# Kernel optimization log

Hardware: AMD Instinct MI355X
Metric: run time of the kernel (lower is better)

Reference implementation:

```python
import jax, jax.numpy as jnp
import numpy as np

B, S, D_IN, D_OUT = 4, 2048, 1024, 1024


def setup_inputs() -> dict:
    key = jax.random.key(0)
    kx, kq, kk, kv = jax.random.split(key, 4)
    scale = 1.0 / np.sqrt(D_IN)
    return {
        "x": jax.random.normal(kx, (B, S, D_IN), dtype=jnp.float32),
        "W_q": jax.random.normal(kq, (D_IN, D_OUT), dtype=jnp.float32) * scale,
        "W_k": jax.random.normal(kk, (D_IN, D_OUT), dtype=jnp.float32) * scale,
        "W_v": jax.random.normal(kv, (D_IN, D_OUT), dtype=jnp.float32) * scale,
    }


def reference(x, W_q, W_k, W_v):
    # QKV projections (Linear without bias): [B,S,D_out]
    q = jnp.einsum("bsd,de->bse", x, W_q)
    k = jnp.einsum("bsd,de->bse", x, W_k)
    v = jnp.einsum("bsd,de->bse", x, W_v)

    # Raw scores [B,S,S], causal mask (strict upper triangle -> -inf),
    # then scale by sqrt(d_k) and softmax, matching the torch order of ops.
    scores = jnp.einsum("bqd,bkd->bqk", q, k)
    seq = scores.shape[-1]
    causal = jnp.triu(jnp.ones((seq, seq), dtype=bool), k=1)
    scores = jnp.where(causal[None, :, :], -jnp.inf, scores)
    attn = jax.nn.softmax(scores / jnp.sqrt(jnp.asarray(q.shape[-1], scores.dtype)), axis=-1)
    # dropout p=0.0 -> identity (eval semantics)
    return jnp.einsum("bqk,bkd->bqd", attn, v)
```

## Files before the change

### kernel.cpp

```cpp
#include <hip/hip_runtime.h>

typedef unsigned short u16;
typedef __bf16 bf16x8 __attribute__((ext_vector_type(8)));
typedef float f32x4 __attribute__((ext_vector_type(4)));

__device__ __forceinline__ u16 f2bf(float f) {
    union { float f; unsigned int u; } v; v.f = f;
    unsigned int u = v.u;
    return (u16)((u + 0x7FFFu + ((u >> 16) & 1u)) >> 16);
}
__device__ __forceinline__ float bf2f(u16 h) {
    union { unsigned int u; float f; } v; v.u = ((unsigned int)h) << 16;
    return v.f;
}

__device__ __forceinline__ void load_lds16(const void* g, void* l) {
    __builtin_amdgcn_global_load_lds(
        (const __attribute__((address_space(1))) unsigned int*)g,
        (__attribute__((address_space(3))) unsigned int*)l,
        16, 0, 0);
}

__global__ void __launch_bounds__(256) cast_x_kernel(const float4* __restrict__ X,
                                                     u16* __restrict__ out) {
    int idx = blockIdx.x * 256 + threadIdx.x;
    float4 v = X[idx];
    ushort4 o;
    o.x = f2bf(v.x); o.y = f2bf(v.y); o.z = f2bf(v.z); o.w = f2bf(v.w);
    *(ushort4*)(out + (size_t)idx * 4) = o;
}

__global__ void __launch_bounds__(256) transpose_w_kernel(
    const float* __restrict__ W0, const float* __restrict__ W1, const float* __restrict__ W2,
    u16* __restrict__ O0, u16* __restrict__ O1, u16* __restrict__ O2) {
    const float* W = (blockIdx.z == 0) ? W0 : (blockIdx.z == 1) ? W1 : W2;
    u16* O = (blockIdx.z == 0) ? O0 : (blockIdx.z == 1) ? O1 : O2;
    __shared__ float tile[32][33];
    int tx = threadIdx.x, ty = threadIdx.y;
    int n0 = blockIdx.x * 32, k0 = blockIdx.y * 32;
    #pragma unroll
    for (int j = 0; j < 32; j += 8)
        tile[ty + j][tx] = W[(size_t)(k0 + ty + j) * 1024 + n0 + tx];
    __syncthreads();
    #pragma unroll
    for (int j = 0; j < 32; j += 8)
        O[(size_t)(n0 + ty + j) * 1024 + k0 + tx] = f2bf(tile[tx][ty + j]);
}

template <int MODE>
__global__ void __launch_bounds__(256) gemm_nt(
    const u16* __restrict__ A, const u16* __restrict__ Bq,
    const u16* __restrict__ Bk, const u16* __restrict__ Bv,
    void* __restrict__ Cq, void* __restrict__ Ck, void* __restrict__ Cv,
    float* __restrict__ rowsum,
    int N, int K, long sA, long sB, long sC, float cscale) {
    int mtile, ntile, z;
    if (MODE == 0) {
        int L = blockIdx.x;
        int c = L & 7, t = (L >> 3) & 7, hi = L >> 6;
        int p = hi * 8 + c;
        z = p >> 6; mtile = p & 63; ntile = t;
    } else if (MODE == 1) {
        int c = blockIdx.x & 7, g = blockIdx.x >> 3;
        z = blockIdx.z;
        if (g <= c)               { mtile = c;     ntile = g; }
        else if (g < 2 * c + 10)  { mtile = c + 8; ntile = g - (c + 1); }
        else return;
    } else {
        int L = blockIdx.x;
        int c = L & 7, x = (L >> 3) & 7, hi = L >> 6;
        int p = hi * 8 + c;
        z = p >> 4; mtile = p & 15; ntile = x;
    }

    const u16* B;
    if (MODE == 0) {
        B = (z == 0) ? Bq : (z == 1) ? Bk : Bv;
    } else {
        B = Bq + (size_t)z * sB;
        A += (size_t)z * sA;
    }

    __shared__ __align__(16) u16 As[2][128 * 32];
    __shared__ __align__(16) u16 Bs[2][128 * 32];

    const int tid = threadIdx.x;
    const int lane = tid & 63;
    const int wave = tid >> 6;
    const int wr = wave >> 1, wc = wave & 1;

    int kiters = K >> 6;
    if (MODE == 3) kiters = (mtile + 1) * 2;

    const int r0 = tid >> 2;
    const int kb = (((tid & 3) ^ ((r0 >> 1) & 3))) * 16;

    const char* gA0 = (const char*)(A + (size_t)(mtile * 128 + r0) * K) + kb;
    const char* gA1 = gA0 + (size_t)64 * K * 2;
    const char* gB0 = (const char*)(B + (size_t)(ntile * 128 + r0) * K) + kb;
    const char* gB1 = gB0 + (size_t)64 * K * 2;

    char* lA = (char*)(&As[0][0]) + tid * 16;
    char* lB = (char*)(&Bs[0][0]) + tid * 16;

    f32x4 acc[4][4] = {};

    const int quad = lane >> 4;
    const int l16 = lane & 15;
    const int ch = quad ^ ((l16 >> 1) & 3);
    const int aoff = (wr * 64 + l16) * 32 + ch * 8;
    const int boff = (wc * 64 + l16) * 32 + ch * 8;

    for (int kt = 0; kt < kiters; ++kt) {
        load_lds16(gA0,      lA);
        load_lds16(gA1,      lA + 4096);
        load_lds16(gA0 + 64, lA + 8192);
        load_lds16(gA1 + 64, lA + 12288);
        load_lds16(gB0,      lB);
        load_lds16(gB1,      lB + 4096);
        load_lds16(gB0 + 64, lB + 8192);
        load_lds16(gB1 + 64, lB + 12288);
        gA0 += 128; gA1 += 128; gB0 += 128; gB1 += 128;
        __syncthreads();

        #pragma unroll
        for (int h = 0; h < 2; ++h) {
            const u16* ap = &As[h][aoff];
            const u16* bp = &Bs[h][boff];
            bf16x8 af[4], bfv[4];
            #pragma unroll
            for (int r = 0; r < 4; ++r) af[r] = *(const bf16x8*)(ap + r * 512);
            #pragma unroll
            for (int c = 0; c < 4; ++c) bfv[c] = *(const bf16x8*)(bp + c * 512);
            #pragma unroll
            for (int r = 0; r < 4; ++r)
                #pragma unroll
                for (int c = 0; c < 4; ++c)
                    acc[r][c] = __builtin_amdgcn_mfma_f32_16x16x32_bf16(af[r], bfv[c], acc[r][c], 0, 0, 0);
        }
        __syncthreads();
    }

    const int grow0 = mtile * 128 + wr * 64 + quad * 4;
    const int gcol0 = ntile * 128 + wc * 64 + l16;

    if (MODE == 0) {
        if (z < 2) {
            u16* C = (u16*)((z == 0) ? Cq : Ck);
            #pragma unroll
            for (int r = 0; r < 4; ++r)
                #pragma unroll
                for (int c = 0; c < 4; ++c)
                    #pragma unroll
                    for (int i = 0; i < 4; ++i)
                        C[(size_t)(grow0 + r * 16 + i) * N + gcol0 + c * 16] =
                            f2bf(acc[r][c][i]);
        } else {
            u16* C = (u16*)Cv;
            #pragma unroll
            for (int r = 0; r < 4; ++r) {
                int m0 = grow0 + r * 16;
                int b = m0 >> 11, s0 = m0 & 2047;
                #pragma unroll
                for (int c = 0; c < 4; ++c) {
                    int d = gcol0 + c * 16;
                    ushort4 o;
                    o.x = f2bf(acc[r][c][0]); o.y = f2bf(acc[r][c][1]);
                    o.z = f2bf(acc[r][c][2]); o.w = f2bf(acc[r][c][3]);
                    *(ushort4*)(C + (size_t)b * (1024 * 2048) + (size_t)d * 2048 + s0) = o;
                }
            }
        }
    } else if (MODE == 1) {
        u16* C = (u16*)Cq + (size_t)z * sC;
        float* rs = rowsum + z * 2048;
        const bool diag = (ntile == mtile);
        float rsum[4][4];
        #pragma unroll
        for (int r = 0; r < 4; ++r)
            #pragma unroll
            for (int i = 0; i < 4; ++i) rsum[r][i] = 0.f;
        #pragma unroll
        for (int r = 0; r < 4; ++r)
            #pragma unroll
            for (int c = 0; c < 4; ++c)
                #pragma unroll
                for (int i = 0; i < 4; ++i) {
                    int grow = grow0 + r * 16 + i;
                    int gcol = gcol0 + c * 16;
                    float e = 0.f;
                    if (!diag || gcol <= grow)
                        e = __expf(acc[r][c][i] * cscale - 12.0f);
                    C[(size_t)grow * N + gcol] = f2bf(e);
                    rsum[r][i] += e;
                }
        #pragma unroll
        for (int r = 0; r < 4; ++r)
            #pragma unroll
            for (int i = 0; i < 4; ++i) {
                float s = rsum[r][i];
                s += __shfl_xor(s, 1, 64);
                s += __shfl_xor(s, 2, 64);
                s += __shfl_xor(s, 4, 64);
                s += __shfl_xor(s, 8, 64);
                if (l16 == 0)
                    atomicAdd(&rs[grow0 + r * 16 + i], s);
            }
    } else {
        float* C = (float*)Cq + (size_t)z * sC;
        const float* rs = rowsum + z * 2048;
        #pragma unroll
        for (int r = 0; r < 4; ++r)
            #pragma unroll
            for (int i = 0; i < 4; ++i) {
                int grow = grow0 + r * 16 + i;
                float inv = 1.0f / rs[grow];
                #pragma unroll
                for (int c = 0; c < 4; ++c)
                    C[(size_t)grow * N + gcol0 + c * 16] = acc[r][c][i] * inv;
            }
    }
}

extern "C" void kernel_launch(void* const* d_in, const int* in_sizes, int n_in,
                              void* d_out, int out_size, void* d_ws, size_t ws_size,
                              hipStream_t stream) {
    const float* x  = (const float*)d_in[0];
    const float* Wq = (const float*)d_in[1];
    const float* Wk = (const float*)d_in[2];
    const float* Wv = (const float*)d_in[3];
    float* out = (float*)d_out;
    char* ws = (char*)d_ws;
    const size_t Mi = 1u << 20;

    u16* xb  = (u16*)(ws);
    u16* WqT = (u16*)(ws + 16 * Mi);
    u16* WkT = (u16*)(ws + 18 * Mi);
    u16* WvT = (u16*)(ws + 20 * Mi);
    u16* Q   = (u16*)(ws + 22 * Mi);
    u16* Kb  = (u16*)(ws + 38 * Mi);
    u16* Vt  = (u16*)(ws + 54 * Mi);
    u16* S   = (u16*)(ws + 70 * Mi);
    float* rowsum = (float*)(ws + 16 * Mi);

    cast_x_kernel<<<8192, 256, 0, stream>>>((const float4*)x, xb);
    transpose_w_kernel<<<dim3(32, 32, 3), dim3(32, 8), 0, stream>>>(
        Wq, Wk, Wv, WqT, WkT, WvT);

    gemm_nt<0><<<dim3(1536, 1, 1), 256, 0, stream>>>(
        xb, WqT, WkT, WvT, Q, Kb, Vt, nullptr, 1024, 1024, 0, 0, 0, 1.f);

    hipMemsetAsync(rowsum, 0, 4 * 2048 * sizeof(float), stream);

    gemm_nt<1><<<dim3(192, 1, 4), 256, 0, stream>>>(
        Q, Kb, nullptr, nullptr, S, nullptr, nullptr, rowsum, 2048, 1024,
        (long)2048 * 1024, (long)2048 * 1024, (long)2048 * 2048, 0.03125f);

    gemm_nt<3><<<dim3(512, 1, 1), 256, 0, stream>>>(
        S, Vt, nullptr, nullptr, out, nullptr, nullptr, rowsum, 1024, 2048,
        (long)2048 * 2048, (long)1024 * 2048, (long)2048 * 1024, 1.f);
}
```

Baseline: 237.5 us.

## Fuse prep kernels, move V projection into QK stage, compute rowsums via MFMA

Merges the x cast and weight transpose into one launch. The V projection moves out of the QK projection launch and into the score launch, which balances work across launches. The atomic rowsum accumulation and its memset are replaced by an extra MFMA against a ones vector inside the PV GEMM. The PV tile order is also reversed so the heaviest causal rows are scheduled first. Together these remove two launches, the atomics and the memset, at the cost of extra MFMA work in the final GEMM and a rowsum taken from bf16-rounded probabilities.

```diff
diff --git a/kernel.cpp b/kernel.cpp
--- a/kernel.cpp
+++ b/kernel.cpp
@@ -8,10 +8,6 @@
     union { float f; unsigned int u; } v; v.f = f;
     unsigned int u = v.u;
     return (u16)((u + 0x7FFFu + ((u >> 16) & 1u)) >> 16);
-}
-__device__ __forceinline__ float bf2f(u16 h) {
-    union { unsigned int u; float f; } v; v.u = ((unsigned int)h) << 16;
-    return v.f;
 }
 
 __device__ __forceinline__ void load_lds16(const void* g, void* l) {
@@ -21,65 +17,84 @@
         16, 0, 0);
 }
 
-__global__ void __launch_bounds__(256) cast_x_kernel(const float4* __restrict__ X,
-                                                     u16* __restrict__ out) {
-    int idx = blockIdx.x * 256 + threadIdx.x;
-    float4 v = X[idx];
-    ushort4 o;
-    o.x = f2bf(v.x); o.y = f2bf(v.y); o.z = f2bf(v.z); o.w = f2bf(v.w);
-    *(ushort4*)(out + (size_t)idx * 4) = o;
-}
-
-__global__ void __launch_bounds__(256) transpose_w_kernel(
-    const float* __restrict__ W0, const float* __restrict__ W1, const float* __restrict__ W2,
-    u16* __restrict__ O0, u16* __restrict__ O1, u16* __restrict__ O2) {
-    const float* W = (blockIdx.z == 0) ? W0 : (blockIdx.z == 1) ? W1 : W2;
-    u16* O = (blockIdx.z == 0) ? O0 : (blockIdx.z == 1) ? O1 : O2;
+__global__ void __launch_bounds__(256) prep_kernel(
+    const float4* __restrict__ X, u16* __restrict__ xb,
+    const float* __restrict__ Wq, const float* __restrict__ Wk,
+    const float* __restrict__ Wv,
+    u16* __restrict__ Oq, u16* __restrict__ Ok, u16* __restrict__ Ov) {
     __shared__ float tile[32][33];
-    int tx = threadIdx.x, ty = threadIdx.y;
-    int n0 = blockIdx.x * 32, k0 = blockIdx.y * 32;
-    #pragma unroll
-    for (int j = 0; j < 32; j += 8)
-        tile[ty + j][tx] = W[(size_t)(k0 + ty + j) * 1024 + n0 + tx];
-    __syncthreads();
-    #pragma unroll
-    for (int j = 0; j < 32; j += 8)
-        O[(size_t)(n0 + ty + j) * 1024 + k0 + tx] = f2bf(tile[tx][ty + j]);
+    const int bid = blockIdx.x, tid = threadIdx.x;
+    if (bid < 8192) {
+        int idx = bid * 256 + tid;
+        float4 v = X[idx];
+        ushort4 o;
+        o.x = f2bf(v.x); o.y = f2bf(v.y); o.z = f2bf(v.z); o.w = f2bf(v.w);
+        *(ushort4*)(xb + (size_t)idx * 4) = o;
+    } else {
+        int id = bid - 8192;
+        int zz = id >> 10;
+        const float* W = (zz == 0) ? Wq : (zz == 1) ? Wk : Wv;
+        u16* O = (zz == 0) ? Oq : (zz == 1) ? Ok : Ov;
+        int n0 = (id & 31) * 32, k0 = ((id >> 5) & 31) * 32;
+        int tx = tid & 31, ty = tid >> 5;
+        #pragma unroll
+        for (int j = 0; j < 32; j += 8)
+            tile[ty + j][tx] = W[(size_t)(k0 + ty + j) * 1024 + n0 + tx];
+        __syncthreads();
+        #pragma unroll
+        for (int j = 0; j < 32; j += 8)
+            O[(size_t)(n0 + ty + j) * 1024 + k0 + tx] = f2bf(tile[tx][ty + j]);
+    }
 }
 
 template <int MODE>
 __global__ void __launch_bounds__(256) gemm_nt(
-    const u16* __restrict__ A, const u16* __restrict__ Bq,
-    const u16* __restrict__ Bk, const u16* __restrict__ Bv,
-    void* __restrict__ Cq, void* __restrict__ Ck, void* __restrict__ Cv,
-    float* __restrict__ rowsum,
-    int N, int K, long sA, long sB, long sC, float cscale) {
+    const u16* __restrict__ xb, const u16* __restrict__ WqT,
+    const u16* __restrict__ WkT, const u16* __restrict__ WvT,
+    u16* __restrict__ Q, u16* __restrict__ Kb,
+    u16* __restrict__ Vt, u16* __restrict__ S,
+    float* __restrict__ out) {
+
     int mtile, ntile, z;
+    const u16 *A, *B;
+    int vsub = 0;
+
     if (MODE == 0) {
         int L = blockIdx.x;
         int c = L & 7, t = (L >> 3) & 7, hi = L >> 6;
         int p = hi * 8 + c;
         z = p >> 6; mtile = p & 63; ntile = t;
+        A = xb;
+        B = z ? WkT : WqT;
     } else if (MODE == 1) {
-        int c = blockIdx.x & 7, g = blockIdx.x >> 3;
-        z = blockIdx.z;
-        if (g <= c)               { mtile = c;     ntile = g; }
-        else if (g < 2 * c + 10)  { mtile = c + 8; ntile = g - (c + 1); }
-        else return;
+        if (blockIdx.x < 512) {
+            vsub = 1;
+            int id = blockIdx.x;
+            int c = id & 7, t = (id >> 3) & 7, hi = id >> 6;
+            mtile = hi * 8 + c; ntile = t; z = 0;
+            A = xb; B = WvT;
+        } else {
+            int id2 = blockIdx.x - 512;
+            z = id2 / 192;
+            int r = id2 - z * 192;
+            int c = r & 7, g = r >> 3;
+            if (g <= c)            { mtile = c;     ntile = g; }
+            else if (g < 2*c + 10) { mtile = c + 8; ntile = g - (c + 1); }
+            else return;
+            A = Q  + (size_t)z * (2048 * 1024);
+            B = Kb + (size_t)z * (2048 * 1024);
+        }
     } else {
         int L = blockIdx.x;
-        int c = L & 7, x = (L >> 3) & 7, hi = L >> 6;
-        int p = hi * 8 + c;
-        z = p >> 4; mtile = p & 15; ntile = x;
-    }
-
-    const u16* B;
-    if (MODE == 0) {
-        B = (z == 0) ? Bq : (z == 1) ? Bk : Bv;
-    } else {
-        B = Bq + (size_t)z * sB;
-        A += (size_t)z * sA;
-    }
+        int c = L & 7, j = (L >> 3) & 7, h = L >> 6;
+        int P = h * 8 + c;
+        z = P & 3; mtile = 15 - (P >> 2); ntile = j;
+        A = S  + (size_t)z * (2048 * 2048);
+        B = Vt + (size_t)z * (1024 * 2048);
+    }
+
+    const int LDA = (MODE == 3) ? 2048 : 1024;
+    const int kiters = (MODE == 3) ? (mtile + 1) * 2 : 16;
 
     __shared__ __align__(16) u16 As[2][128 * 32];
     __shared__ __align__(16) u16 Bs[2][128 * 32];
@@ -89,21 +104,23 @@
     const int wave = tid >> 6;
     const int wr = wave >> 1, wc = wave & 1;
 
-    int kiters = K >> 6;
-    if (MODE == 3) kiters = (mtile + 1) * 2;
-
     const int r0 = tid >> 2;
     const int kb = (((tid & 3) ^ ((r0 >> 1) & 3))) * 16;
 
-    const char* gA0 = (const char*)(A + (size_t)(mtile * 128 + r0) * K) + kb;
-    const char* gA1 = gA0 + (size_t)64 * K * 2;
-    const char* gB0 = (const char*)(B + (size_t)(ntile * 128 + r0) * K) + kb;
-    const char* gB1 = gB0 + (size_t)64 * K * 2;
+    const char* gA0 = (const char*)(A + (size_t)(mtile * 128 + r0) * LDA) + kb;
+    const char* gA1 = gA0 + (size_t)64 * LDA * 2;
+    const char* gB0 = (const char*)(B + (size_t)(ntile * 128 + r0) * LDA) + kb;
+    const char* gB1 = gB0 + (size_t)64 * LDA * 2;
 
     char* lA = (char*)(&As[0][0]) + tid * 16;
     char* lB = (char*)(&Bs[0][0]) + tid * 16;
 
     f32x4 acc[4][4] = {};
+    f32x4 acc_rs[4] = {};
+
+    bf16x8 vones;
+    #pragma unroll
+    for (int i = 0; i < 8; ++i) vones[i] = (__bf16)1.0f;
 
     const int quad = lane >> 4;
     const int l16 = lane & 15;
@@ -124,19 +141,26 @@
         __syncthreads();
 
         #pragma unroll
-        for (int h = 0; h < 2; ++h) {
-            const u16* ap = &As[h][aoff];
-            const u16* bp = &Bs[h][boff];
+        for (int h2 = 0; h2 < 2; ++h2) {
+            const u16* ap = &As[h2][aoff];
+            const u16* bp = &Bs[h2][boff];
             bf16x8 af[4], bfv[4];
             #pragma unroll
             for (int r = 0; r < 4; ++r) af[r] = *(const bf16x8*)(ap + r * 512);
             #pragma unroll
             for (int c = 0; c < 4; ++c) bfv[c] = *(const bf16x8*)(bp + c * 512);
+            if (MODE == 3) {
+                #pragma unroll
+                for (int r = 0; r < 4; ++r)
+                    acc_rs[r] = __builtin_amdgcn_mfma_f32_16x16x32_bf16(
+                        af[r], vones, acc_rs[r], 0, 0, 0);
+            }
             #pragma unroll
             for (int r = 0; r < 4; ++r)
                 #pragma unroll
                 for (int c = 0; c < 4; ++c)
-                    acc[r][c] = __builtin_amdgcn_mfma_f32_16x16x32_bf16(af[r], bfv[c], acc[r][c], 0, 0, 0);
+                    acc[r][c] = __builtin_amdgcn_mfma_f32_16x16x32_bf16(
+                        af[r], bfv[c], acc[r][c], 0, 0, 0);
         }
         __syncthreads();
     }
@@ -145,18 +169,17 @@
     const int gcol0 = ntile * 128 + wc * 64 + l16;
 
     if (MODE == 0) {
-        if (z < 2) {
-            u16* C = (u16*)((z == 0) ? Cq : Ck);
-            #pragma unroll
-            for (int r = 0; r < 4; ++r)
-                #pragma unroll
-                for (int c = 0; c < 4; ++c)
-                    #pragma unroll
-                    for (int i = 0; i < 4; ++i)
-                        C[(size_t)(grow0 + r * 16 + i) * N + gcol0 + c * 16] =
-                            f2bf(acc[r][c][i]);
-        } else {
-            u16* C = (u16*)Cv;
+        u16* C = z ? Kb : Q;
+        #pragma unroll
+        for (int r = 0; r < 4; ++r)
+            #pragma unroll
+            for (int c = 0; c < 4; ++c)
+                #pragma unroll
+                for (int i = 0; i < 4; ++i)
+                    C[(size_t)(grow0 + r * 16 + i) * 1024 + gcol0 + c * 16] =
+                        f2bf(acc[r][c][i]);
+    } else if (MODE == 1) {
+        if (vsub) {
             #pragma unroll
             for (int r = 0; r < 4; ++r) {
                 int m0 = grow0 + r * 16;
@@ -167,57 +190,37 @@
                     ushort4 o;
                     o.x = f2bf(acc[r][c][0]); o.y = f2bf(acc[r][c][1]);
                     o.z = f2bf(acc[r][c][2]); o.w = f2bf(acc[r][c][3]);
-                    *(ushort4*)(C + (size_t)b * (1024 * 2048) + (size_t)d * 2048 + s0) = o;
+                    *(ushort4*)(Vt + (size_t)b * (1024 * 2048) + (size_t)d * 2048 + s0) = o;
                 }
             }
+        } else {
+            u16* C = S + (size_t)z * (2048 * 2048);
+            const bool diag = (ntile == mtile);
+            #pragma unroll
+            for (int r = 0; r < 4; ++r)
+                #pragma unroll
+                for (int c = 0; c < 4; ++c)
+                    #pragma unroll
+                    for (int i = 0; i < 4; ++i) {
+                        int grow = grow0 + r * 16 + i;
+                        int gcol = gcol0 + c * 16;
+                        float e = 0.f;
+                        if (!diag || gcol <= grow)
+                            e = __expf(acc[r][c][i] * 0.03125f - 12.0f);
+                        C[(size_t)grow * 2048 + gcol] = f2bf(e);
+                    }
         }
-    } else if (MODE == 1) {
-        u16* C = (u16*)Cq + (size_t)z * sC;
-        float* rs = rowsum + z * 2048;
-        const bool diag = (ntile == mtile);
-        float rsum[4][4];
-        #pragma unroll
-        for (int r = 0; r < 4; ++r)
-            #pragma unroll
-            for (int i = 0; i < 4; ++i) rsum[r][i] = 0.f;
-        #pragma unroll
-        for (int r = 0; r < 4; ++r)
-            #pragma unroll
-            for (int c = 0; c < 4; ++c)
-                #pragma unroll
-                for (int i = 0; i < 4; ++i) {
-                    int grow = grow0 + r * 16 + i;
-                    int gcol = gcol0 + c * 16;
-                    float e = 0.f;
-                    if (!diag || gcol <= grow)
-                        e = __expf(acc[r][c][i] * cscale - 12.0f);
-                    C[(size_t)grow * N + gcol] = f2bf(e);
-                    rsum[r][i] += e;
-                }
-        #pragma unroll
-        for (int r = 0; r < 4; ++r)
-            #pragma unroll
-            for (int i = 0; i < 4; ++i) {
-                float s = rsum[r][i];
-                s += __shfl_xor(s, 1, 64);
-                s += __shfl_xor(s, 2, 64);
-                s += __shfl_xor(s, 4, 64);
-                s += __shfl_xor(s, 8, 64);
-                if (l16 == 0)
-                    atomicAdd(&rs[grow0 + r * 16 + i], s);
-            }
     } else {
-        float* C = (float*)Cq + (size_t)z * sC;
-        const float* rs = rowsum + z * 2048;
+        float* C = out + (size_t)z * (2048 * 1024);
         #pragma unroll
         for (int r = 0; r < 4; ++r)
             #pragma unroll
             for (int i = 0; i < 4; ++i) {
                 int grow = grow0 + r * 16 + i;
-                float inv = 1.0f / rs[grow];
+                float inv = 1.0f / acc_rs[r][i];
                 #pragma unroll
                 for (int c = 0; c < 4; ++c)
-                    C[(size_t)grow * N + gcol0 + c * 16] = acc[r][c][i] * inv;
+                    C[(size_t)grow * 1024 + gcol0 + c * 16] = acc[r][c][i] * inv;
             }
     }
 }
@@ -241,22 +244,13 @@
     u16* Kb  = (u16*)(ws + 38 * Mi);
     u16* Vt  = (u16*)(ws + 54 * Mi);
     u16* S   = (u16*)(ws + 70 * Mi);
-    float* rowsum = (float*)(ws + 16 * Mi);
-
-    cast_x_kernel<<<8192, 256, 0, stream>>>((const float4*)x, xb);
-    transpose_w_kernel<<<dim3(32, 32, 3), dim3(32, 8), 0, stream>>>(
-        Wq, Wk, Wv, WqT, WkT, WvT);
-
-    gemm_nt<0><<<dim3(1536, 1, 1), 256, 0, stream>>>(
-        xb, WqT, WkT, WvT, Q, Kb, Vt, nullptr, 1024, 1024, 0, 0, 0, 1.f);
-
-    hipMemsetAsync(rowsum, 0, 4 * 2048 * sizeof(float), stream);
-
-    gemm_nt<1><<<dim3(192, 1, 4), 256, 0, stream>>>(
-        Q, Kb, nullptr, nullptr, S, nullptr, nullptr, rowsum, 2048, 1024,
-        (long)2048 * 1024, (long)2048 * 1024, (long)2048 * 2048, 0.03125f);
-
-    gemm_nt<3><<<dim3(512, 1, 1), 256, 0, stream>>>(
-        S, Vt, nullptr, nullptr, out, nullptr, nullptr, rowsum, 1024, 2048,
-        (long)2048 * 2048, (long)1024 * 2048, (long)2048 * 1024, 1.f);
-}
+
+    prep_kernel<<<11264, 256, 0, stream>>>(
+        (const float4*)x, xb, Wq, Wk, Wv, WqT, WkT, WvT);
+
+    gemm_nt<0><<<1024, 256, 0, stream>>>(xb, WqT, WkT, WvT, Q, Kb, Vt, S, out);
+
+    gemm_nt<1><<<1280, 256, 0, stream>>>(xb, WqT, WkT, WvT, Q, Kb, Vt, S, out);
+
+    gemm_nt<3><<<512, 256, 0, stream>>>(xb, WqT, WkT, WvT, Q, Kb, Vt, S, out);
+}
```

Measured after the change: 231.1 us. -2.7%, faster.
